# Kernel optimization log

Hardware: AMD Instinct MI355X
Metric: run time of the kernel (lower is better)

Reference implementation:

```python
import jax, jax.numpy as jnp
import numpy as np

B, S, C = 16, 2048, 1024
H = 8            # preference_dim / num_heads
HD = C // H      # head_dim = 128


def setup_inputs() -> dict:
    key = jax.random.key(0)
    ks = jax.random.split(key, 8)
    s1 = 1.0 / np.sqrt(1.0)   # Linear(1, HD) init scale (not critical)
    sh = 1.0 / np.sqrt(HD)
    return {
        "features": jax.random.normal(ks[0], (B, S, C), dtype=jnp.float32),
        "preference": jax.random.normal(ks[1], (B, H), dtype=jnp.float32),
        "Wq": jax.random.uniform(ks[2], (HD, 1), jnp.float32, -s1, s1),
        "bq": jax.random.uniform(ks[3], (HD,), jnp.float32, -s1, s1),
        "Wk": jax.random.uniform(ks[4], (HD, HD), jnp.float32, -sh, sh),
        "bk": jax.random.uniform(ks[5], (HD,), jnp.float32, -sh, sh),
        "Wv": jax.random.uniform(ks[6], (HD, HD), jnp.float32, -sh, sh),
        "bv": jax.random.uniform(ks[7], (HD,), jnp.float32, -sh, sh),
    }


def reference(features, preference, Wq, bq, Wk, bk, Wv, bv):
    b, s, c = features.shape
    h, hd = H, HD
    # query: Linear(1->hd) applied to per-head scalar preference; constant over step
    # q[b,h,d] = preference[b,h] * Wq[d,0] + bq[d]
    q = preference[:, :, None] * Wq[:, 0][None, None, :] + bq  # [B,H,HD]
    f = features.reshape(b, s, h, hd)                          # head slices
    k = jnp.einsum('bshd,ed->bshe', f, Wk) + bk                # [B,S,H,HD]
    v = jnp.einsum('bshd,ed->bshe', f, Wv) + bv                # [B,S,H,HD]
    # original builds [B,S,S] scores per head, but query rows are identical
    # across step, so softmax(q @ k^T) @ v has identical rows; compute once.
    scores = jnp.einsum('bhd,bshd->bhs', q, k)                 # [B,H,S]
    attn = jax.nn.softmax(scores, axis=-1)
    ctx = jnp.einsum('bhs,bshd->bhd', attn, v)                 # [B,H,HD]
    weighted = jnp.broadcast_to(ctx[:, None, :, :], (b, s, h, hd)).reshape(b, s, c)
    return weighted + features
```

## Files before the change

kernel.cpp:

```cpp
#include <hip/hip_runtime.h>
#include <math.h>

#define B 16
#define S 2048
#define C 1024
#define H 8
#define HD 128
#define NC 64
#define R (S / NC)

__global__ __launch_bounds__(256) void k2_pass(
    const float* __restrict__ feat, const float* __restrict__ pref,
    const float* __restrict__ Wq, const float* __restrict__ bq,
    const float* __restrict__ Wk,
    float* __restrict__ pm, float* __restrict__ pl, float* __restrict__ pf) {
    int wg    = blockIdx.x;
    int b     = wg >> 6;
    int chunk = wg & (NC - 1);
    int t     = threadIdx.x;
    int h     = t >> 5;
    int lane32 = t & 31;

    float p = pref[b * H + h];
    float4 qv; qv.x = qv.y = qv.z = qv.w = 0.f;
    const float4* Wk4 = (const float4*)Wk;
#pragma unroll 8
    for (int e = 0; e < HD; ++e) {
        float qe = p * Wq[e] + bq[e];
        float4 w = Wk4[e * (HD / 4) + lane32];
        qv.x += qe * w.x; qv.y += qe * w.y;
        qv.z += qe * w.z; qv.w += qe * w.w;
    }

    const float4* frow = (const float4*)feat
                       + (size_t)(b * S + chunk * R) * (C / 4) + t;
    float m = -1e30f, l = 0.f;
    float4 a; a.x = a.y = a.z = a.w = 0.f;

#pragma unroll
    for (int s0 = 0; s0 < R; s0 += 4) {
        float4 f[4]; float sc[4];
#pragma unroll
        for (int j = 0; j < 4; ++j)
            f[j] = frow[(size_t)(s0 + j) * (C / 4)];
#pragma unroll
        for (int j = 0; j < 4; ++j) {
            float part = f[j].x * qv.x + f[j].y * qv.y
                       + f[j].z * qv.z + f[j].w * qv.w;
            part += __shfl_xor(part, 16, 32);
            part += __shfl_xor(part, 8, 32);
            part += __shfl_xor(part, 4, 32);
            part += __shfl_xor(part, 2, 32);
            part += __shfl_xor(part, 1, 32);
            sc[j] = part;
        }
#pragma unroll
        for (int j = 0; j < 4; ++j) {
            float mn    = fmaxf(m, sc[j]);
            float scale = __expf(m - mn);
            float pw    = __expf(sc[j] - mn);
            l   = l * scale + pw;
            a.x = a.x * scale + pw * f[j].x;
            a.y = a.y * scale + pw * f[j].y;
            a.z = a.z * scale + pw * f[j].z;
            a.w = a.w * scale + pw * f[j].w;
            m   = mn;
        }
    }
    if (lane32 == 0) { pm[wg * H + h] = m; pl[wg * H + h] = l; }
    ((float4*)pf)[(size_t)wg * (C / 4) + t] = a;
}

__global__ __launch_bounds__(128) void k3_combine(
    const float* __restrict__ pm, const float* __restrict__ pl,
    const float* __restrict__ pf, const float* __restrict__ Wv,
    const float* __restrict__ bv, float* __restrict__ ctx) {
    int bh = blockIdx.x;
    int b = bh >> 3, h = bh & 7;
    int t = threadIdx.x;
    __shared__ float wsh[NC];
    __shared__ float fsh[HD];

    float M = -1e30f;
#pragma unroll 8
    for (int i = 0; i < NC; ++i)
        M = fmaxf(M, pm[(b * NC + i) * H + h]);
    if (t < NC) wsh[t] = __expf(pm[(b * NC + t) * H + h] - M);
    __syncthreads();
    float L = 0.f;
#pragma unroll 8
    for (int i = 0; i < NC; ++i)
        L += pl[(b * NC + i) * H + h] * wsh[i];
    float acc = 0.f;
#pragma unroll 8
    for (int i = 0; i < NC; ++i)
        acc += pf[(size_t)(b * NC + i) * C + h * HD + t] * wsh[i];
    fsh[t] = acc / L;
    __syncthreads();
    float s = 0.f;
#pragma unroll 8
    for (int d = 0; d < HD; ++d)
        s += fsh[d] * Wv[t * HD + d];
    ctx[bh * HD + t] = s + bv[t];
}

__global__ __launch_bounds__(256) void k4_epilogue(
    const float* __restrict__ feat, const float* __restrict__ ctx,
    float* __restrict__ out) {
    constexpr int N4 = B * S * C / 4;
    int tid = blockIdx.x * 256 + threadIdx.x;
    int nth = gridDim.x * 256;
    for (int i = tid; i < N4; i += nth) {
        float4 f = ((const float4*)feat)[i];
        int b  = i >> 19;
        int c4 = i & 255;
        float4 cv = ((const float4*)ctx)[b * (C / 4) + c4];
        float4 o; o.x = f.x + cv.x; o.y = f.y + cv.y;
        o.z = f.z + cv.z; o.w = f.w + cv.w;
        ((float4*)out)[i] = o;
    }
}

extern "C" void kernel_launch(void* const* d_in, const int* in_sizes, int n_in,
                              void* d_out, int out_size, void* d_ws, size_t ws_size,
                              hipStream_t stream) {
    const float* feat = (const float*)d_in[0];
    const float* pref = (const float*)d_in[1];
    const float* Wq   = (const float*)d_in[2];
    const float* bq   = (const float*)d_in[3];
    const float* Wk   = (const float*)d_in[4];
    const float* Wv   = (const float*)d_in[6];
    const float* bv   = (const float*)d_in[7];
    float* out = (float*)d_out;

    float* ws  = (float*)d_ws;
    float* ctx = ws;
    float* pm  = ctx + B * C;
    float* pl  = pm + B * NC * H;
    float* pf  = pl + B * NC * H;

    k2_pass<<<B * NC, 256, 0, stream>>>(feat, pref, Wq, bq, Wk, pm, pl, pf);
    k3_combine<<<B * H, 128, 0, stream>>>(pm, pl, pf, Wv, bv, ctx);
    k4_epilogue<<<4096, 256, 0, stream>>>(feat, ctx, out);
}
```

Measured before the change: 318.4 us.

## Hoist q·Wk into separate kernel, widen chunk split, use nontemporal epilogue

Moves the per-head q·Wk projection out of every k2 workgroup into a small k1 kernel, so the streaming pass no longer recomputes it. The number of chunks per batch grows from 64 to 256, and each workgroup loads all 8 rows up front and does a two-pass max-then-exp softmax in place of the online rescaling. The combine kernel stages the partial max and sum values in shared memory to handle the larger partial count. The epilogue uses nontemporal loads and stores. The trade-off is one extra launch and more partial traffic for k3 to reduce.

```diff
diff --git a/kernel.cpp b/kernel.cpp
--- a/kernel.cpp
+++ b/kernel.cpp
@@ -6,68 +6,73 @@
 #define C 1024
 #define H 8
 #define HD 128
-#define NC 64
+#define NC 256
 #define R (S / NC)
 
+typedef float vf4 __attribute__((ext_vector_type(4)));
+
+__global__ __launch_bounds__(128) void k1_qk(
+    const float* __restrict__ pref, const float* __restrict__ Wq,
+    const float* __restrict__ bq, const float* __restrict__ Wk,
+    float* __restrict__ qk) {
+    int bh = blockIdx.x;
+    int d  = threadIdx.x;
+    __shared__ float qsh[HD];
+    float p = pref[bh];
+    qsh[d] = p * Wq[d] + bq[d];
+    __syncthreads();
+    float s = 0.f;
+#pragma unroll 8
+    for (int e = 0; e < HD; ++e)
+        s += qsh[e] * Wk[e * HD + d];
+    qk[bh * HD + d] = s;
+}
+
 __global__ __launch_bounds__(256) void k2_pass(
-    const float* __restrict__ feat, const float* __restrict__ pref,
-    const float* __restrict__ Wq, const float* __restrict__ bq,
-    const float* __restrict__ Wk,
+    const float* __restrict__ feat, const float* __restrict__ qk,
     float* __restrict__ pm, float* __restrict__ pl, float* __restrict__ pf) {
-    int wg    = blockIdx.x;
-    int b     = wg >> 6;
-    int chunk = wg & (NC - 1);
-    int t     = threadIdx.x;
-    int h     = t >> 5;
+    int wg     = blockIdx.x;
+    int b      = wg >> 8;
+    int chunk  = wg & (NC - 1);
+    int t      = threadIdx.x;
+    int h      = t >> 5;
     int lane32 = t & 31;
-
-    float p = pref[b * H + h];
-    float4 qv; qv.x = qv.y = qv.z = qv.w = 0.f;
-    const float4* Wk4 = (const float4*)Wk;
-#pragma unroll 8
-    for (int e = 0; e < HD; ++e) {
-        float qe = p * Wq[e] + bq[e];
-        float4 w = Wk4[e * (HD / 4) + lane32];
-        qv.x += qe * w.x; qv.y += qe * w.y;
-        qv.z += qe * w.z; qv.w += qe * w.w;
-    }
 
     const float4* frow = (const float4*)feat
                        + (size_t)(b * S + chunk * R) * (C / 4) + t;
-    float m = -1e30f, l = 0.f;
+    float4 qv = ((const float4*)qk)[(b * H + h) * (HD / 4) + lane32];
+
+    float4 f[R];
+#pragma unroll
+    for (int i = 0; i < R; ++i)
+        f[i] = frow[(size_t)i * (C / 4)];
+
+    float sc[R];
+#pragma unroll
+    for (int i = 0; i < R; ++i) {
+        float p = f[i].x * qv.x + f[i].y * qv.y + f[i].z * qv.z + f[i].w * qv.w;
+        p += __shfl_xor(p, 16, 32);
+        p += __shfl_xor(p, 8, 32);
+        p += __shfl_xor(p, 4, 32);
+        p += __shfl_xor(p, 2, 32);
+        p += __shfl_xor(p, 1, 32);
+        sc[i] = p;
+    }
+
+    float M = sc[0];
+#pragma unroll
+    for (int i = 1; i < R; ++i) M = fmaxf(M, sc[i]);
+
+    float l = 0.f;
     float4 a; a.x = a.y = a.z = a.w = 0.f;
-
 #pragma unroll
-    for (int s0 = 0; s0 < R; s0 += 4) {
-        float4 f[4]; float sc[4];
-#pragma unroll
-        for (int j = 0; j < 4; ++j)
-            f[j] = frow[(size_t)(s0 + j) * (C / 4)];
-#pragma unroll
-        for (int j = 0; j < 4; ++j) {
-            float part = f[j].x * qv.x + f[j].y * qv.y
-                       + f[j].z * qv.z + f[j].w * qv.w;
-            part += __shfl_xor(part, 16, 32);
-            part += __shfl_xor(part, 8, 32);
-            part += __shfl_xor(part, 4, 32);
-            part += __shfl_xor(part, 2, 32);
-            part += __shfl_xor(part, 1, 32);
-            sc[j] = part;
-        }
-#pragma unroll
-        for (int j = 0; j < 4; ++j) {
-            float mn    = fmaxf(m, sc[j]);
-            float scale = __expf(m - mn);
-            float pw    = __expf(sc[j] - mn);
-            l   = l * scale + pw;
-            a.x = a.x * scale + pw * f[j].x;
-            a.y = a.y * scale + pw * f[j].y;
-            a.z = a.z * scale + pw * f[j].z;
-            a.w = a.w * scale + pw * f[j].w;
-            m   = mn;
-        }
+    for (int i = 0; i < R; ++i) {
+        float w = __expf(sc[i] - M);
+        l   += w;
+        a.x += w * f[i].x; a.y += w * f[i].y;
+        a.z += w * f[i].z; a.w += w * f[i].w;
     }
-    if (lane32 == 0) { pm[wg * H + h] = m; pl[wg * H + h] = l; }
+    if (lane32 == 0) { pm[wg * H + h] = M; pl[wg * H + h] = l; }
     ((float4*)pf)[(size_t)wg * (C / 4) + t] = a;
 }
 
@@ -78,23 +83,27 @@
     int bh = blockIdx.x;
     int b = bh >> 3, h = bh & 7;
     int t = threadIdx.x;
-    __shared__ float wsh[NC];
-    __shared__ float fsh[HD];
+    __shared__ float wm[NC], wl[NC], we[NC], fsh[HD];
 
+#pragma unroll
+    for (int i = t; i < NC; i += 128) {
+        wm[i] = pm[(b * NC + i) * H + h];
+        wl[i] = pl[(b * NC + i) * H + h];
+    }
+    __syncthreads();
     float M = -1e30f;
 #pragma unroll 8
-    for (int i = 0; i < NC; ++i)
-        M = fmaxf(M, pm[(b * NC + i) * H + h]);
-    if (t < NC) wsh[t] = __expf(pm[(b * NC + t) * H + h] - M);
+    for (int i = 0; i < NC; ++i) M = fmaxf(M, wm[i]);
+#pragma unroll
+    for (int i = t; i < NC; i += 128) we[i] = __expf(wm[i] - M);
     __syncthreads();
     float L = 0.f;
 #pragma unroll 8
-    for (int i = 0; i < NC; ++i)
-        L += pl[(b * NC + i) * H + h] * wsh[i];
+    for (int i = 0; i < NC; ++i) L += wl[i] * we[i];
     float acc = 0.f;
 #pragma unroll 8
     for (int i = 0; i < NC; ++i)
-        acc += pf[(size_t)(b * NC + i) * C + h * HD + t] * wsh[i];
+        acc += we[i] * pf[(size_t)(b * NC + i) * C + h * HD + t];
     fsh[t] = acc / L;
     __syncthreads();
     float s = 0.f;
@@ -111,13 +120,12 @@
     int tid = blockIdx.x * 256 + threadIdx.x;
     int nth = gridDim.x * 256;
     for (int i = tid; i < N4; i += nth) {
-        float4 f = ((const float4*)feat)[i];
+        vf4 f = __builtin_nontemporal_load((const vf4*)feat + i);
         int b  = i >> 19;
         int c4 = i & 255;
-        float4 cv = ((const float4*)ctx)[b * (C / 4) + c4];
-        float4 o; o.x = f.x + cv.x; o.y = f.y + cv.y;
-        o.z = f.z + cv.z; o.w = f.w + cv.w;
-        ((float4*)out)[i] = o;
+        vf4 cv = *((const vf4*)ctx + b * (C / 4) + c4);
+        vf4 o = f + cv;
+        __builtin_nontemporal_store(o, (vf4*)out + i);
     }
 }
 
@@ -134,12 +142,14 @@
     float* out = (float*)d_out;
 
     float* ws  = (float*)d_ws;
-    float* ctx = ws;
+    float* qk  = ws;
+    float* ctx = qk + B * H * HD;
     float* pm  = ctx + B * C;
     float* pl  = pm + B * NC * H;
     float* pf  = pl + B * NC * H;
 
-    k2_pass<<<B * NC, 256, 0, stream>>>(feat, pref, Wq, bq, Wk, pm, pl, pf);
+    k1_qk<<<B * H, 128, 0, stream>>>(pref, Wq, bq, Wk, qk);
+    k2_pass<<<B * NC, 256, 0, stream>>>(feat, qk, pm, pl, pf);
     k3_combine<<<B * H, 128, 0, stream>>>(pm, pl, pf, Wv, bv, ctx);
     k4_epilogue<<<4096, 256, 0, stream>>>(feat, ctx, out);
 }
```

Result: faster. 298.3 us (-6.3%).
